# Optimization experiments

Measured on AMD Instinct MI355X. Metric: run time of the kernel, lower is better.

The kernel has to match this reference:

```python
import jax, jax.numpy as jnp
import numpy as np

N_NODES = 50000
N_EDGES = 1600000
IN_F = 512
OUT_F = 256


def setup_inputs() -> dict:
    key = jax.random.key(0)
    k1, k2, k3, k4, k5 = jax.random.split(key, 5)
    features = jax.random.normal(k1, (N_NODES, IN_F), dtype=jnp.float32)
    # xavier_uniform init for weight [in_features, out_features]
    limit = np.sqrt(6.0 / (IN_F + OUT_F)).astype(np.float32)
    weight = jax.random.uniform(k2, (IN_F, OUT_F), dtype=jnp.float32,
                                minval=-limit, maxval=limit)
    # COO sparse adjacency (normalized edge weights in [0,1))
    edge_vals = jax.random.uniform(k3, (N_EDGES,), dtype=jnp.float32)
    edge_rows = jax.random.randint(k4, (N_EDGES,), 0, N_NODES, dtype=jnp.int32)
    edge_cols = jax.random.randint(k5, (N_EDGES,), 0, N_NODES, dtype=jnp.int32)
    return {"features": features, "weight": weight, "edge_vals": edge_vals,
            "edge_rows": edge_rows, "edge_cols": edge_cols}


def reference(features, weight, edge_vals, edge_rows, edge_cols):
    # dropout p=0.0 / eval mode -> identity
    support = features @ weight                      # [N, out_f] dense GEMM
    # torch.spmm(adj, support): out[r] += val * support[c] for each edge (r, c)
    gathered = support[edge_cols] * edge_vals[:, None]   # [E, out_f]
    output = jax.ops.segment_sum(gathered, edge_rows, num_segments=N_NODES)
    return jax.nn.relu(output)
```

## Files before the change

### kernel.cpp

```cpp
#include <hip/hip_runtime.h>

#define N_NODES 50000
#define N_EDGES 1600000
#define IN_F    512
#define OUT_F   256

#define BROWS   128
#define NBINS   ((N_NODES + BROWS - 1) / BROWS)
#define BATCH   2048
#define NBATCHES ((N_EDGES + BATCH - 1) / BATCH)

typedef __attribute__((ext_vector_type(8))) short bf16x8;
typedef __attribute__((ext_vector_type(4))) float f32x4;

__device__ __forceinline__ short bf16rne(float f) {
    unsigned u = __builtin_bit_cast(unsigned, f);
    u += 0x7fffu + ((u >> 16) & 1u);
    return (short)(u >> 16);
}

__device__ __forceinline__ float b2f(unsigned short h) {
    unsigned u = (unsigned)h << 16;
    return __builtin_bit_cast(float, u);
}

__global__ __launch_bounds__(256) void wt_kernel(const float* __restrict__ W,
                                                 short* __restrict__ Wt) {
    int idx = blockIdx.x * 256 + threadIdx.x;
    if (idx < IN_F * OUT_F) {
        int n = idx >> 9;
        int k = idx & 511;
        Wt[idx] = bf16rne(W[(size_t)k * OUT_F + n]);
    }
}

#define ASTRIDE 40
#define BSTRIDE 40

__global__ __launch_bounds__(512) void gemm_mfma_kernel(const float* __restrict__ A,
                                                        const short* __restrict__ Wt,
                                                        unsigned short* __restrict__ Cb) {
    __shared__ short As[128 * ASTRIDE];
    __shared__ short Bs[256 * BSTRIDE];

    const int tid  = threadIdx.x;
    const int wave = tid >> 6;
    const int lane = tid & 63;
    const int m0   = blockIdx.x * 128;
    const int wrow = (wave >> 2) * 64;
    const int wcol = (wave & 3) * 64;

    const int quad = lane >> 4;
    const int l16  = lane & 15;

    const int ar = tid >> 2;
    const int aq = tid & 3;

    const int bn = tid >> 1;
    const int bh = tid & 1;

    f32x4 zero4 = {0.f, 0.f, 0.f, 0.f};
    f32x4 acc[4][4];
#pragma unroll
    for (int i = 0; i < 4; ++i)
#pragma unroll
        for (int j = 0; j < 4; ++j) acc[i][j] = zero4;

    for (int k0 = 0; k0 < IN_F; k0 += 32) {
        {
            const int gm = m0 + ar;
            float4 v0 = make_float4(0.f, 0.f, 0.f, 0.f);
            float4 v1 = v0;
            if (gm < N_NODES) {
                const float* p = A + (size_t)gm * IN_F + k0 + aq * 8;
                v0 = *(const float4*)p;
                v1 = *(const float4*)(p + 4);
            }
            bf16x8 b;
            b[0] = bf16rne(v0.x); b[1] = bf16rne(v0.y);
            b[2] = bf16rne(v0.z); b[3] = bf16rne(v0.w);
            b[4] = bf16rne(v1.x); b[5] = bf16rne(v1.y);
            b[6] = bf16rne(v1.z); b[7] = bf16rne(v1.w);
            *(bf16x8*)&As[ar * ASTRIDE + aq * 8] = b;
        }
        {
            const short* src = Wt + (size_t)bn * IN_F + k0 + bh * 16;
            bf16x8 w0 = *(const bf16x8*)(src + 0);
            bf16x8 w1 = *(const bf16x8*)(src + 8);
            short* dst = &Bs[bn * BSTRIDE + bh * 16];
            *(bf16x8*)(dst + 0) = w0;
            *(bf16x8*)(dst + 8) = w1;
        }
        __syncthreads();

        bf16x8 af[4], bf[4];
#pragma unroll
        for (int mt = 0; mt < 4; ++mt)
            af[mt] = *(const bf16x8*)&As[(wrow + mt * 16 + l16) * ASTRIDE + quad * 8];
#pragma unroll
        for (int nt = 0; nt < 4; ++nt)
            bf[nt] = *(const bf16x8*)&Bs[(wcol + nt * 16 + l16) * BSTRIDE + quad * 8];

#pragma unroll
        for (int mt = 0; mt < 4; ++mt)
#pragma unroll
            for (int nt = 0; nt < 4; ++nt)
                acc[mt][nt] = __builtin_amdgcn_mfma_f32_16x16x32_bf16(
                    af[mt], bf[nt], acc[mt][nt], 0, 0, 0);
        __syncthreads();
    }

#pragma unroll
    for (int mt = 0; mt < 4; ++mt) {
        const int rbase = m0 + wrow + mt * 16 + quad * 4;
#pragma unroll
        for (int i = 0; i < 4; ++i) {
            const int row = rbase + i;
            if (row < N_NODES) {
#pragma unroll
                for (int nt = 0; nt < 4; ++nt)
                    Cb[(size_t)row * OUT_F + wcol + nt * 16 + l16] =
                        (unsigned short)bf16rne(acc[mt][nt][i]);
            }
        }
    }
}

__global__ __launch_bounds__(256) void zero_bins_kernel(int* __restrict__ binCounts) {
    int i = blockIdx.x * 256 + threadIdx.x;
    if (i < NBINS) binCounts[i] = 0;
}

__global__ __launch_bounds__(256) void histA_kernel(const int* __restrict__ rows,
                                                    int* __restrict__ binCounts) {
    __shared__ int lh[NBINS];
    const int tid = threadIdx.x;
    for (int i = tid; i < NBINS; i += 256) lh[i] = 0;
    __syncthreads();
    for (int i = blockIdx.x * 256 + tid; i < N_EDGES; i += gridDim.x * 256)
        atomicAdd(&lh[rows[i] >> 7], 1);
    __syncthreads();
    for (int i = tid; i < NBINS; i += 256)
        if (lh[i]) atomicAdd(&binCounts[i], lh[i]);
}

__global__ __launch_bounds__(256) void scanA_kernel(const int* __restrict__ binCounts,
                                                    int* __restrict__ binStart,
                                                    int* __restrict__ gcursor) {
    __shared__ int stmp[256];
    const int tid = threadIdx.x;
    const int i0 = 2 * tid, i1 = 2 * tid + 1;
    const int a0 = (i0 < NBINS) ? binCounts[i0] : 0;
    const int a1 = (i1 < NBINS) ? binCounts[i1] : 0;
    const int pair = a0 + a1;
    stmp[tid] = pair;
    for (int off = 1; off < 256; off <<= 1) {
        __syncthreads();
        int t = (tid >= off) ? stmp[tid - off] : 0;
        __syncthreads();
        stmp[tid] += t;
    }
    __syncthreads();
    const int pexcl = stmp[tid] - pair;
    if (i0 < NBINS) { binStart[i0] = pexcl;      gcursor[i0] = pexcl; }
    if (i1 < NBINS) { binStart[i1] = pexcl + a0; gcursor[i1] = pexcl + a0; }
}

__global__ __launch_bounds__(256) void fillA_kernel(const int* __restrict__ rows,
                                                    const int* __restrict__ cols,
                                                    const float* __restrict__ vals,
                                                    int* __restrict__ gcursor,
                                                    int2* __restrict__ binned) {
    __shared__ int lhist[NBINS];
    __shared__ int lexcl[NBINS];
    __shared__ int gbase[NBINS];
    __shared__ int stmp[256];
    __shared__ int2 lstage[BATCH];
    __shared__ unsigned short sbucket[BATCH];

    const int tid   = threadIdx.x;
    const int start = blockIdx.x * BATCH;
    const int count = min(BATCH, N_EDGES - start);

    for (int i = tid; i < NBINS; i += 256) lhist[i] = 0;
    __syncthreads();

    int myrow[8], myrank[8];
#pragma unroll
    for (int j = 0; j < 8; ++j) {
        const int s = j * 256 + tid;
        if (s < count) {
            const int r = rows[start + s];
            myrow[j]  = r;
            myrank[j] = atomicAdd(&lhist[r >> 7], 1);
        }
    }
    __syncthreads();

    {
        const int i0 = 2 * tid, i1 = 2 * tid + 1;
        const int a0 = (i0 < NBINS) ? lhist[i0] : 0;
        const int a1 = (i1 < NBINS) ? lhist[i1] : 0;
        const int pair = a0 + a1;
        stmp[tid] = pair;
        for (int off = 1; off < 256; off <<= 1) {
            __syncthreads();
            int t = (tid >= off) ? stmp[tid - off] : 0;
            __syncthreads();
            stmp[tid] += t;
        }
        __syncthreads();
        const int pexcl = stmp[tid] - pair;
        if (i0 < NBINS) {
            lexcl[i0] = pexcl;
            gbase[i0] = a0 ? atomicAdd(&gcursor[i0], a0) : 0;
        }
        if (i1 < NBINS) {
            lexcl[i1] = pexcl + a0;
            gbase[i1] = a1 ? atomicAdd(&gcursor[i1], a1) : 0;
        }
    }
    __syncthreads();

#pragma unroll
    for (int j = 0; j < 8; ++j) {
        const int s = j * 256 + tid;
        if (s < count) {
            const int r   = myrow[j];
            const int b   = r >> 7;
            const int pos = lexcl[b] + myrank[j];
            lstage[pos]  = make_int2(((r & 127) << 16) | cols[start + s],
                                     __float_as_int(vals[start + s]));
            sbucket[pos] = (unsigned short)b;
        }
    }
    __syncthreads();

#pragma unroll
    for (int j = 0; j < 8; ++j) {
        const int s = j * 256 + tid;
        if (s < count) {
            const int b = sbucket[s];
            binned[gbase[b] + (s - lexcl[b])] = lstage[s];
        }
    }
}

__global__ __launch_bounds__(256) void sortB_kernel(const int2* __restrict__ binned,
                                                    const int* __restrict__ binStart,
                                                    const int* __restrict__ binCounts,
                                                    int* __restrict__ excl,
                                                    unsigned int* __restrict__ ecv) {
    __shared__ int lhist[BROWS];
    __shared__ int lcur[BROWS];

    const int tid  = threadIdx.x;
    const int b    = blockIdx.x;
    const int base = binStart[b];
    const int cnt  = binCounts[b];

    if (tid < BROWS) lhist[tid] = 0;
    __syncthreads();

    for (int i = tid; i < cnt; i += 256)
        atomicAdd(&lhist[binned[base + i].x >> 16], 1);
    __syncthreads();

    if (tid < BROWS) lcur[tid] = lhist[tid];
    for (int off = 1; off < BROWS; off <<= 1) {
        __syncthreads();
        int t = (tid >= off && tid < BROWS) ? lcur[tid - off] : 0;
        __syncthreads();
        if (tid < BROWS) lcur[tid] += t;
    }
    __syncthreads();
    if (tid < BROWS) {
        const int pexcl = lcur[tid] - lhist[tid];
        const int row   = b * BROWS + tid;
        lcur[tid] = pexcl;
        if (row < N_NODES) excl[row] = base + pexcl;
    }
    __syncthreads();

    for (int i = tid; i < cnt; i += 256) {
        const int2 e  = binned[base + i];
        const int rl  = e.x >> 16;
        const int col = e.x & 0xFFFF;
        const int rank = atomicAdd(&lcur[rl], 1);
        ecv[base + rank] = ((unsigned int)col << 16) |
                           (unsigned short)bf16rne(__int_as_float(e.y));
    }
}

__global__ __launch_bounds__(256) void gather_kernel(const ushort4* __restrict__ support,
                                                     const int* __restrict__ excl,
                                                     const unsigned int* __restrict__ ecv,
                                                     float4* __restrict__ out) {
    const int tid  = threadIdx.x;
    const int row  = blockIdx.x * 4 + (tid >> 6);
    const int lane = tid & 63;
    if (row >= N_NODES) return;

    const int start = excl[row];
    const int end   = (row + 1 < N_NODES) ? excl[row + 1] : N_EDGES;

    float4 acc = make_float4(0.f, 0.f, 0.f, 0.f);
    int e = start;
    const int end4 = start + ((end - start) & ~3);
    for (; e < end4; e += 4) {
        const unsigned int p0 = ecv[e];
        const unsigned int p1 = ecv[e + 1];
        const unsigned int p2 = ecv[e + 2];
        const unsigned int p3 = ecv[e + 3];
        const ushort4 s0 = support[(size_t)(p0 >> 16) * 64 + lane];
        const ushort4 s1 = support[(size_t)(p1 >> 16) * 64 + lane];
        const ushort4 s2 = support[(size_t)(p2 >> 16) * 64 + lane];
        const ushort4 s3 = support[(size_t)(p3 >> 16) * 64 + lane];
        const float v0 = b2f((unsigned short)(p0 & 0xFFFF));
        const float v1 = b2f((unsigned short)(p1 & 0xFFFF));
        const float v2 = b2f((unsigned short)(p2 & 0xFFFF));
        const float v3 = b2f((unsigned short)(p3 & 0xFFFF));
        acc.x += v0 * b2f(s0.x); acc.y += v0 * b2f(s0.y);
        acc.z += v0 * b2f(s0.z); acc.w += v0 * b2f(s0.w);
        acc.x += v1 * b2f(s1.x); acc.y += v1 * b2f(s1.y);
        acc.z += v1 * b2f(s1.z); acc.w += v1 * b2f(s1.w);
        acc.x += v2 * b2f(s2.x); acc.y += v2 * b2f(s2.y);
        acc.z += v2 * b2f(s2.z); acc.w += v2 * b2f(s2.w);
        acc.x += v3 * b2f(s3.x); acc.y += v3 * b2f(s3.y);
        acc.z += v3 * b2f(s3.z); acc.w += v3 * b2f(s3.w);
    }
    for (; e < end; ++e) {
        const unsigned int p0 = ecv[e];
        const ushort4 s0 = support[(size_t)(p0 >> 16) * 64 + lane];
        const float v0 = b2f((unsigned short)(p0 & 0xFFFF));
        acc.x += v0 * b2f(s0.x); acc.y += v0 * b2f(s0.y);
        acc.z += v0 * b2f(s0.z); acc.w += v0 * b2f(s0.w);
    }

    acc.x = fmaxf(acc.x, 0.f);
    acc.y = fmaxf(acc.y, 0.f);
    acc.z = fmaxf(acc.z, 0.f);
    acc.w = fmaxf(acc.w, 0.f);
    out[(size_t)row * 64 + lane] = acc;
}

extern "C" void kernel_launch(void* const* d_in, const int* in_sizes, int n_in,
                              void* d_out, int out_size, void* d_ws, size_t ws_size,
                              hipStream_t stream) {
    const float* features  = (const float*)d_in[0];
    const float* weight    = (const float*)d_in[1];
    const float* edge_vals = (const float*)d_in[2];
    const int*   edge_rows = (const int*)d_in[3];
    const int*   edge_cols = (const int*)d_in[4];
    float* out = (float*)d_out;

    unsigned short* support_bf = (unsigned short*)d_ws;
    int2*  binned    = (int2*)(support_bf + (size_t)N_NODES * OUT_F);
    unsigned int* ecv = (unsigned int*)(binned + N_EDGES);
    int*   excl      = (int*)(ecv + N_EDGES);
    int*   binCounts = excl + N_NODES;
    int*   binStart  = binCounts + 512;
    int*   gcursor   = binStart + 512;
    short* Wt        = (short*)(gcursor + 512);

    wt_kernel<<<(IN_F * OUT_F + 255) / 256, 256, 0, stream>>>(weight, Wt);

    gemm_mfma_kernel<<<(N_NODES + 127) / 128, 512, 0, stream>>>(features, Wt, support_bf);

    zero_bins_kernel<<<2, 256, 0, stream>>>(binCounts);
    histA_kernel<<<256, 256, 0, stream>>>(edge_rows, binCounts);
    scanA_kernel<<<1, 256, 0, stream>>>(binCounts, binStart, gcursor);
    fillA_kernel<<<NBATCHES, 256, 0, stream>>>(edge_rows, edge_cols, edge_vals,
                                               gcursor, binned);
    sortB_kernel<<<NBINS, 256, 0, stream>>>(binned, binStart, binCounts, excl, ecv);

    gather_kernel<<<(N_NODES + 3) / 4, 256, 0, stream>>>(
        (const ushort4*)support_bf, excl, ecv, (float4*)out);
}
```

Baseline: 369.4 us.

## Fold global bin scan into fill kernel, double batch size, widen sort blocks

Removes the separate single-block scan kernel. Each fill block now recomputes the global bin prefix sum alongside its local histogram scan, packing both into one 64-bit scan, and takes its slot through relative per-bin atomic cursors. The fill batch grows from 2048 to 4096 edges per block and the sort kernel runs with 512 threads. This saves one launch and one serialization point, at the cost of redundant scan work in every fill block and more shared memory per block.

```diff
diff --git a/kernel.cpp b/kernel.cpp
--- a/kernel.cpp
+++ b/kernel.cpp
@@ -7,11 +7,13 @@
 
 #define BROWS   128
 #define NBINS   ((N_NODES + BROWS - 1) / BROWS)
-#define BATCH   2048
+#define BATCH   4096
 #define NBATCHES ((N_EDGES + BATCH - 1) / BATCH)
+#define EPT     (BATCH / 256)
 
 typedef __attribute__((ext_vector_type(8))) short bf16x8;
 typedef __attribute__((ext_vector_type(4))) float f32x4;
+typedef unsigned long long ull;
 
 __device__ __forceinline__ short bf16rne(float f) {
     unsigned u = __builtin_bit_cast(unsigned, f);
@@ -126,9 +128,10 @@
     }
 }
 
-__global__ __launch_bounds__(256) void zero_bins_kernel(int* __restrict__ binCounts) {
+__global__ __launch_bounds__(256) void zero_bins_kernel(int* __restrict__ binCounts,
+                                                        int* __restrict__ relCur) {
     int i = blockIdx.x * 256 + threadIdx.x;
-    if (i < NBINS) binCounts[i] = 0;
+    if (i < NBINS) { binCounts[i] = 0; relCur[i] = 0; }
 }
 
 __global__ __launch_bounds__(256) void histA_kernel(const int* __restrict__ rows,
@@ -144,37 +147,17 @@
         if (lh[i]) atomicAdd(&binCounts[i], lh[i]);
 }
 
-__global__ __launch_bounds__(256) void scanA_kernel(const int* __restrict__ binCounts,
-                                                    int* __restrict__ binStart,
-                                                    int* __restrict__ gcursor) {
-    __shared__ int stmp[256];
-    const int tid = threadIdx.x;
-    const int i0 = 2 * tid, i1 = 2 * tid + 1;
-    const int a0 = (i0 < NBINS) ? binCounts[i0] : 0;
-    const int a1 = (i1 < NBINS) ? binCounts[i1] : 0;
-    const int pair = a0 + a1;
-    stmp[tid] = pair;
-    for (int off = 1; off < 256; off <<= 1) {
-        __syncthreads();
-        int t = (tid >= off) ? stmp[tid - off] : 0;
-        __syncthreads();
-        stmp[tid] += t;
-    }
-    __syncthreads();
-    const int pexcl = stmp[tid] - pair;
-    if (i0 < NBINS) { binStart[i0] = pexcl;      gcursor[i0] = pexcl; }
-    if (i1 < NBINS) { binStart[i1] = pexcl + a0; gcursor[i1] = pexcl + a0; }
-}
-
 __global__ __launch_bounds__(256) void fillA_kernel(const int* __restrict__ rows,
                                                     const int* __restrict__ cols,
                                                     const float* __restrict__ vals,
-                                                    int* __restrict__ gcursor,
+                                                    const int* __restrict__ binCounts,
+                                                    int* __restrict__ relCur,
+                                                    int* __restrict__ binStart,
                                                     int2* __restrict__ binned) {
     __shared__ int lhist[NBINS];
     __shared__ int lexcl[NBINS];
     __shared__ int gbase[NBINS];
-    __shared__ int stmp[256];
+    __shared__ ull stmp2[256];
     __shared__ int2 lstage[BATCH];
     __shared__ unsigned short sbucket[BATCH];
 
@@ -185,9 +168,9 @@
     for (int i = tid; i < NBINS; i += 256) lhist[i] = 0;
     __syncthreads();
 
-    int myrow[8], myrank[8];
-#pragma unroll
-    for (int j = 0; j < 8; ++j) {
+    int myrow[EPT], myrank[EPT];
+#pragma unroll
+    for (int j = 0; j < EPT; ++j) {
         const int s = j * 256 + tid;
         if (s < count) {
             const int r = rows[start + s];
@@ -199,31 +182,37 @@
 
     {
         const int i0 = 2 * tid, i1 = 2 * tid + 1;
-        const int a0 = (i0 < NBINS) ? lhist[i0] : 0;
-        const int a1 = (i1 < NBINS) ? lhist[i1] : 0;
-        const int pair = a0 + a1;
-        stmp[tid] = pair;
+        const int h0 = (i0 < NBINS) ? lhist[i0] : 0;
+        const int h1 = (i1 < NBINS) ? lhist[i1] : 0;
+        const int c0 = (i0 < NBINS) ? binCounts[i0] : 0;
+        const int c1 = (i1 < NBINS) ? binCounts[i1] : 0;
+        const ull pair = ((ull)(unsigned)(c0 + c1) << 32) | (unsigned)(h0 + h1);
+        stmp2[tid] = pair;
         for (int off = 1; off < 256; off <<= 1) {
             __syncthreads();
-            int t = (tid >= off) ? stmp[tid - off] : 0;
+            ull t = (tid >= off) ? stmp2[tid - off] : 0ull;
             __syncthreads();
-            stmp[tid] += t;
-        }
-        __syncthreads();
-        const int pexcl = stmp[tid] - pair;
+            stmp2[tid] += t;
+        }
+        __syncthreads();
+        const ull pex  = stmp2[tid] - pair;
+        const int lex0 = (int)(pex & 0xffffffffull);
+        const int bst0 = (int)(pex >> 32);
         if (i0 < NBINS) {
-            lexcl[i0] = pexcl;
-            gbase[i0] = a0 ? atomicAdd(&gcursor[i0], a0) : 0;
+            lexcl[i0] = lex0;
+            gbase[i0] = bst0 + (h0 ? atomicAdd(&relCur[i0], h0) : 0);
+            if (blockIdx.x == 0) binStart[i0] = bst0;
         }
         if (i1 < NBINS) {
-            lexcl[i1] = pexcl + a0;
-            gbase[i1] = a1 ? atomicAdd(&gcursor[i1], a1) : 0;
-        }
-    }
-    __syncthreads();
-
-#pragma unroll
-    for (int j = 0; j < 8; ++j) {
+            lexcl[i1] = lex0 + h0;
+            gbase[i1] = (bst0 + c0) + (h1 ? atomicAdd(&relCur[i1], h1) : 0);
+            if (blockIdx.x == 0) binStart[i1] = bst0 + c0;
+        }
+    }
+    __syncthreads();
+
+#pragma unroll
+    for (int j = 0; j < EPT; ++j) {
         const int s = j * 256 + tid;
         if (s < count) {
             const int r   = myrow[j];
@@ -237,7 +226,7 @@
     __syncthreads();
 
 #pragma unroll
-    for (int j = 0; j < 8; ++j) {
+    for (int j = 0; j < EPT; ++j) {
         const int s = j * 256 + tid;
         if (s < count) {
             const int b = sbucket[s];
@@ -246,7 +235,7 @@
     }
 }
 
-__global__ __launch_bounds__(256) void sortB_kernel(const int2* __restrict__ binned,
+__global__ __launch_bounds__(512) void sortB_kernel(const int2* __restrict__ binned,
                                                     const int* __restrict__ binStart,
                                                     const int* __restrict__ binCounts,
                                                     int* __restrict__ excl,
@@ -262,7 +251,7 @@
     if (tid < BROWS) lhist[tid] = 0;
     __syncthreads();
 
-    for (int i = tid; i < cnt; i += 256)
+    for (int i = tid; i < cnt; i += 512)
         atomicAdd(&lhist[binned[base + i].x >> 16], 1);
     __syncthreads();
 
@@ -282,7 +271,7 @@
     }
     __syncthreads();
 
-    for (int i = tid; i < cnt; i += 256) {
+    for (int i = tid; i < cnt; i += 512) {
         const int2 e  = binned[base + i];
         const int rl  = e.x >> 16;
         const int col = e.x & 0xFFFF;
@@ -360,19 +349,18 @@
     int*   excl      = (int*)(ecv + N_EDGES);
     int*   binCounts = excl + N_NODES;
     int*   binStart  = binCounts + 512;
-    int*   gcursor   = binStart + 512;
-    short* Wt        = (short*)(gcursor + 512);
+    int*   relCur    = binStart + 512;
+    short* Wt        = (short*)(relCur + 512);
 
     wt_kernel<<<(IN_F * OUT_F + 255) / 256, 256, 0, stream>>>(weight, Wt);
 
     gemm_mfma_kernel<<<(N_NODES + 127) / 128, 512, 0, stream>>>(features, Wt, support_bf);
 
-    zero_bins_kernel<<<2, 256, 0, stream>>>(binCounts);
+    zero_bins_kernel<<<2, 256, 0, stream>>>(binCounts, relCur);
     histA_kernel<<<256, 256, 0, stream>>>(edge_rows, binCounts);
-    scanA_kernel<<<1, 256, 0, stream>>>(binCounts, binStart, gcursor);
     fillA_kernel<<<NBATCHES, 256, 0, stream>>>(edge_rows, edge_cols, edge_vals,
-                                               gcursor, binned);
-    sortB_kernel<<<NBINS, 256, 0, stream>>>(binned, binStart, binCounts, excl, ecv);
+                                               binCounts, relCur, binStart, binned);
+    sortB_kernel<<<NBINS, 512, 0, stream>>>(binned, binStart, binCounts, excl, ecv);
 
     gather_kernel<<<(N_NODES + 3) / 4, 256, 0, stream>>>(
         (const ushort4*)support_bf, excl, ecv, (float4*)out);
```

Result: faster. 353.2 us (-4.4%).
